# Performance work log

Hardware: AMD Instinct MI355X
Metric: run time of the kernel (lower is better)

The kernel has to match this reference:

```python
import jax, jax.numpy as jnp
import numpy as np

T, B, D, H = 512, 128, 512, 512

def setup_inputs() -> dict:
    key = jax.random.key(0)
    k1, k2, k3, k4 = jax.random.split(key, 4)
    s_in = 1.0 / np.sqrt(D)
    s_h = 1.0 / np.sqrt(H)
    return {
        "x": jax.random.normal(k1, (T, B, D), dtype=jnp.float32),
        "resets": jax.random.randint(k2, (T, B), 0, 2) > 0,
        "h0": jnp.zeros((B, H), dtype=jnp.float32),  # GRUCell.initialize_carry -> zeros
        "Wi": jax.random.normal(k3, (D, 3 * H), dtype=jnp.float32) * s_in,  # [ir|iz|in]
        "bi": jnp.zeros((3 * H,), dtype=jnp.float32),
        "Wh": jax.random.normal(k4, (H, 3 * H), dtype=jnp.float32) * s_h,  # [hr|hz|hn]
        "bhn": jnp.zeros((H,), dtype=jnp.float32),
    }

def reference(x, resets, h0, Wi, bi, Wh, bhn):
    # Precompute all input-side gate projections in one big GEMM: [T,B,3H]
    xg = jnp.einsum('tbd,dk->tbk', x, Wi) + bi

    def step(h, inp):
        xg_t, reset_t = inp
        # reset masking: replace carry with fresh zero carry where episode resets
        h = jnp.where(reset_t[:, None], jnp.zeros_like(h), h)
        hg = h @ Wh  # [B,3H]
        xr, xz, xn = jnp.split(xg_t, 3, axis=-1)
        hr, hz, hn = jnp.split(hg, 3, axis=-1)
        r = jax.nn.sigmoid(xr + hr)
        z = jax.nn.sigmoid(xz + hz)
        n = jnp.tanh(xn + r * (hn + bhn))
        h_new = (1.0 - z) * n + z * h
        return h_new, h_new

    h_final, ys = jax.lax.scan(step, h0, (xg, resets))
    return h_final, ys
```

## Files before the change

### kernel.cpp

```cpp
#include <hip/hip_runtime.h>

typedef __attribute__((ext_vector_type(4))) float f32x4;
typedef __attribute__((ext_vector_type(8))) _Float16 f16x8;
typedef __attribute__((ext_vector_type(4))) _Float16 f16x4;
typedef unsigned short u16;
typedef unsigned int u32;
typedef unsigned long long u64;

#define XGCAP 36864

__device__ __forceinline__ float sigm(float v){ return 1.0f / (1.0f + __expf(-v)); }
__device__ __forceinline__ float tanh_fast(float v){
  v = fminf(15.0f, fmaxf(-15.0f, v));
  float e = __expf(2.0f * v);
  return (e - 1.0f) / (e + 1.0f);
}
__device__ __forceinline__ void gload16(const void* g, void* l){
  __builtin_amdgcn_global_load_lds((const __attribute__((address_space(1))) void*)g,
                                   (__attribute__((address_space(3))) void*)l, 16, 0, 0);
}
__device__ __forceinline__ double aload(const double* p){
  return __hip_atomic_load(p, __ATOMIC_RELAXED, __HIP_MEMORY_SCOPE_AGENT);
}
__device__ __forceinline__ void astore(float* p, float v){
  __hip_atomic_store(p, v, __ATOMIC_RELAXED, __HIP_MEMORY_SCOPE_AGENT);
}
__device__ __forceinline__ float2 d2f2(double d){ union{double d; float2 f;} u; u.d = d; return u.f; }

__global__ __launch_bounds__(512) void prep_lists(
    const void* __restrict__ resets_raw,
    u32* __restrict__ rows, u32* __restrict__ off, int* __restrict__ nlists)
{
  __shared__ u32 bitmap[2048];
  __shared__ u32 cnt[520];
  __shared__ u32 offs[521];
  __shared__ u32 cur[520];
  __shared__ int is_bytes;
  const int tid = threadIdx.x;
  const int lane = tid & 63, wave = tid >> 6;
  for (int i = tid; i < 2048; i += 512) bitmap[i] = 0;
  for (int i = tid; i < 520; i += 512){ cnt[i] = 0; cur[i] = 0; }
  if (tid == 0) is_bytes = 0;
  for (int i = tid; i < 64; i += 512) rows[65536 + i] = (2u << 16);
  __syncthreads();
  {
    const u32* w = (const u32*)resets_raw;
    int bad = 0;
    for (int i = tid; i < 4096; i += 512) bad |= (w[i] > 1u);
    if (bad) atomicOr(&is_bytes, 1);
  }
  __syncthreads();
  if (is_bytes){
    const u32* wb = (const u32*)resets_raw;
    for (int i = tid; i < 16384; i += 512){
      u32 v = wb[i];
      u32 bits = ((v & 0xFFu) ? 1u : 0u) | (((v >> 8) & 0xFFu) ? 2u : 0u)
               | (((v >> 16) & 0xFFu) ? 4u : 0u) | (((v >> 24) & 0xFFu) ? 8u : 0u);
      if (bits) atomicOr(&bitmap[i >> 3], bits << ((i & 7) * 4));
    }
  } else {
    const u32* w = (const u32*)resets_raw;
    for (int r = 0; r < 128; ++r){
      u32 v = w[r * 512 + tid];
      u64 m = __ballot(v != 0u);
      if (lane == 0){
        int idx = r * 16 + wave * 2;
        bitmap[idx]     = (u32)m;
        bitmap[idx + 1] = (u32)(m >> 32);
      }
    }
  }
  __syncthreads();
  if (tid < 128){
    const int b = tid;
    int depth = 0;
    for (int t = 0; t < 512; ++t){
      int pos = t * 128 + b;
      bool rs = (bitmap[pos >> 5] >> (pos & 31)) & 1u;
      depth = rs ? 0 : ((t == 0) ? 0 : depth + 1);
      int li = (depth == 0) ? (rs ? 0 : 1) : (depth + 1);
      atomicAdd(&cnt[li], 1u);
    }
  }
  __syncthreads();
  if (tid == 0){
    u32 s = 0; int mx = 0;
    for (int i = 0; i < 520; ++i){
      offs[i] = s; s += cnt[i];
      if (cnt[i]) mx = i;
    }
    offs[520] = s;
    *nlists = mx + 1;
  }
  __syncthreads();
  for (int i = tid; i < 521; i += 512) off[i] = offs[i];
  __syncthreads();
  if (tid < 128){
    const int b = tid;
    int depth = 0;
    for (int t = 0; t < 512; ++t){
      int pos = t * 128 + b;
      bool rs = (bitmap[pos >> 5] >> (pos & 31)) & 1u;
      depth = rs ? 0 : ((t == 0) ? 0 : depth + 1);
      int li = (depth == 0) ? (rs ? 0 : 1) : (depth + 1);
      u32 p = offs[li] + atomicAdd(&cur[li], 1u);
      u32 fl = rs ? 1u : ((t == 0) ? 2u : 0u);
      rows[p] = (u32)t | ((u32)b << 9) | (fl << 16);
    }
  }
}

__global__ void prep_w(const float* __restrict__ Wi, const float* __restrict__ Wh,
                       char* __restrict__ wimg)
{
  __shared__ float tile[64][65];
  const int bc = blockIdx.x % 24;
  const int bk = blockIdx.x / 24;
  const int scol0 = (bc % 3) * 512 + (bc / 3) * 64;
  const int k0 = bk * 64;
  #pragma unroll
  for (int i = 0; i < 4; ++i){
    int idx = (int)threadIdx.x + i*256;
    int kk = idx >> 4, c4 = idx & 15;
    int k = k0 + kk;
    const float* src = (k < 512) ? (Wi + (size_t)k*1536 + scol0 + c4*4)
                                 : (Wh + (size_t)(k-512)*1536 + scol0 + c4*4);
    float4 v = *(const float4*)src;
    tile[kk][c4*4+0] = v.x; tile[kk][c4*4+1] = v.y;
    tile[kk][c4*4+2] = v.z; tile[kk][c4*4+3] = v.w;
  }
  __syncthreads();
  const int jb = bc / 3;
  #pragma unroll
  for (int i = 0; i < 4; ++i){
    int idx = (int)threadIdx.x + i*256;
    int cc = idx >> 4, k4 = idx & 15;
    int cimg = (bc % 3)*64 + cc;
    f16x4 c;
    c[0] = (_Float16)tile[k4*4+0][cc]; c[1] = (_Float16)tile[k4*4+1][cc];
    c[2] = (_Float16)tile[k4*4+2][cc]; c[3] = (_Float16)tile[k4*4+3][cc];
    int bby = k4*8;
    int sb = (bby & 8) | ((bby & 0x70) ^ ((cimg & 7) << 4));
    *(f16x4*)(wimg + ((size_t)(jb*16 + bk))*24576 + cimg*128 + sb) = c;
  }
}

__global__ __launch_bounds__(256, 2) void xg_gemm(
    const float* __restrict__ x, const float* __restrict__ bi,
    const float* __restrict__ bhn, const char* __restrict__ wimg,
    _Float16* __restrict__ xg, const u32* __restrict__ rows,
    const u32* __restrict__ off, u32* __restrict__ flags,
    float* __restrict__ out)
{
  __shared__ __align__(16) char smem[81920];
  const int tid = threadIdx.x;
  const int lane = tid & 63, wave = tid >> 6;
  const int c_  = (int)blockIdx.x & 7;
  const int q_  = (int)blockIdx.x >> 3;
  const int jblk = q_ & 7;
  const int tm = c_ + ((q_ >> 3) << 3);
  float* ys = out + 65536;
  const u32 n0 = off[1];
  const size_t wbase = ((size_t)jblk*16)*24576;

  const float* rp[8];
  #pragma unroll
  for (int i = 0; i < 8; ++i){
    u32 e = rows[tm*128 + (tid>>4) + i*16];
    rp[i] = x + ((size_t)((e & 511u)*128u + ((e >> 9) & 127u)))*512 + (tid & 15)*4;
  }

  f32x4 acc[3][8];
  #pragma unroll
  for (int c = 0; c < 3; ++c)
    #pragma unroll
    for (int m = 0; m < 8; ++m) acc[c][m] = (f32x4){0.f,0.f,0.f,0.f};

  float4 areg[8];
  #pragma unroll
  for (int i = 0; i < 8; ++i) areg[i] = *(const float4*)(rp[i]);
  {
    const char* g = wimg + wbase + wave*6144 + lane*16;
    char* l = smem + 32768 + wave*6144;
    #pragma unroll
    for (int i = 0; i < 6; ++i) gload16(g + i*1024, l + i*1024);
  }
  #pragma unroll
  for (int i = 0; i < 8; ++i){
    int r = (tid>>4) + i*16, bby = (tid & 15)*8;
    int sb = (bby & 8) | ((bby & 0x70) ^ ((r & 7) << 4));
    f16x4 c; c[0]=(_Float16)areg[i].x; c[1]=(_Float16)areg[i].y;
             c[2]=(_Float16)areg[i].z; c[3]=(_Float16)areg[i].w;
    *(f16x4*)(smem + r*128 + sb) = c;
  }
  __syncthreads();

  for (int kc = 0; kc < 8; ++kc){
    const int cur = kc & 1;
    if (kc < 7){
      #pragma unroll
      for (int i = 0; i < 8; ++i) areg[i] = *(const float4*)(rp[i] + (kc+1)*64);
      const char* g = wimg + wbase + (size_t)(kc+1)*24576 + wave*6144 + lane*16;
      char* l = smem + 32768 + ((kc+1)&1)*24576 + wave*6144;
      #pragma unroll
      for (int i = 0; i < 6; ++i) gload16(g + i*1024, l + i*1024);
    }
    const char* Ab = smem + cur*16384;
    const char* Wb = smem + 32768 + cur*24576;
    #pragma unroll
    for (int kk = 0; kk < 2; ++kk){
      const int bby = kk*64 + (lane>>4)*16;
      f16x8 af[8];
      #pragma unroll
      for (int mi = 0; mi < 8; ++mi){
        int rr = mi*16 + (lane & 15);
        af[mi] = *(const f16x8*)(Ab + rr*128 + (bby ^ ((rr & 7) << 4)));
      }
      #pragma unroll
      for (int cls = 0; cls < 3; ++cls){
        int cc = cls*64 + wave*16 + (lane & 15);
        f16x8 wf = *(const f16x8*)(Wb + cc*128 + (bby ^ ((cc & 7) << 4)));
        #pragma unroll
        for (int mi = 0; mi < 8; ++mi)
          acc[cls][mi] = __builtin_amdgcn_mfma_f32_16x16x32_f16(af[mi], wf, acc[cls][mi], 0, 0, 0);
      }
    }
    if (kc < 7){
      char* An = smem + ((kc+1)&1)*16384;
      #pragma unroll
      for (int i = 0; i < 8; ++i){
        int r = (tid>>4) + i*16, bby = (tid & 15)*8;
        int sb = (bby & 8) | ((bby & 0x70) ^ ((r & 7) << 4));
        f16x4 c; c[0]=(_Float16)areg[i].x; c[1]=(_Float16)areg[i].y;
                 c[2]=(_Float16)areg[i].z; c[3]=(_Float16)areg[i].w;
        *(f16x4*)(An + r*128 + sb) = c;
      }
    }
    __syncthreads();
  }

  const int jloc = wave*16 + (lane & 15);
  const int j = jblk*64 + jloc;
  const float bir = bi[j], biz = bi[512 + j], bin = bi[1024 + j], bh = bhn[j];
  #pragma unroll
  for (int mi = 0; mi < 8; ++mi){
    #pragma unroll
    for (int rg = 0; rg < 4; ++rg){
      int r = mi*16 + (lane >> 4)*4 + rg;
      u32 e = rows[tm*128 + r];
      int tt = (int)(e & 511u), bb = (int)((e >> 9) & 127u);
      float xr = acc[0][mi][rg] + bir;
      float xz = acc[1][mi][rg] + biz;
      float xn = acc[2][mi][rg] + bin;
      if ((e >> 16) == 1u){
        float rr = sigm(xr), zz = sigm(xz);
        float nn = tanh_fast(xn + rr*bh);
        ys[((size_t)(tt*128 + bb))*512 + j] = (1.f - zz)*nn;
      } else {
        u32 xi = (u32)(tm*128 + r) - n0;
        if (xi >= XGCAP) xi = 0;
        _Float16* p = xg + (size_t)xi*1536 + jblk*192 + jloc;
        p[0]   = (_Float16)xr;
        p[64]  = (_Float16)xz;
        p[128] = (_Float16)xn;
      }
    }
  }
  __syncthreads();
  if (tid < 128){
    u32 e = rows[tm*128 + tid];
    if ((e >> 16) == 1u){
      u32 fidx = (e & 511u)*128u + ((e >> 9) & 127u);
      __hip_atomic_fetch_add(&flags[fidx], 1u, __ATOMIC_RELAXED, __HIP_MEMORY_SCOPE_AGENT);
    }
  }
}

__global__ __launch_bounds__(256, 2) void gru_scan(
    const float* __restrict__ h0, const float* __restrict__ bhn,
    const char* __restrict__ wimg, const _Float16* __restrict__ xg,
    const u32* __restrict__ rows, const u32* __restrict__ off,
    const int* __restrict__ nlists, u32* __restrict__ flags,
    float* __restrict__ out)
{
  __shared__ __align__(16) char smem[32768];
  float* ys = out + 65536;
  const int L = *nlists;
  const u32 n0 = off[1];
  const int tid = threadIdx.x;
  const int lane = tid & 63, wave = tid >> 6;
  const int nblk = (int)gridDim.x;

  int myNext = (int)blockIdx.x;
  int gt = 0;
  for (int li = 1; li < L; ++li){
    const u32 offA = off[li];
    const int nA = (int)(off[li+1] - offA);
    const int tA = (nA + 63) >> 6;
    const int nt = tA * 8;
    while (myNext < gt + nt){
      const int tile = myNext - gt;
      myNext += nblk;
      const int tm = tile >> 3, jb = tile & 7;
      const u32 rowbase = offA + (u32)tm*64u;
      const int mcount = min(64, nA - tm*64);
      const char* wp = wimg + ((size_t)jb*16 + 8)*24576;
      const int jloc = wave*16 + (lane & 15);

      if (wave == 0){
        u32 e = rows[rowbase + lane];
        if (lane < mcount && (e >> 16) == 0u){
          u32 fidx = ((e & 511u) - 1u)*128u + ((e >> 9) & 127u);
          int guard = 0;
          while (__hip_atomic_load(&flags[fidx], __ATOMIC_RELAXED, __HIP_MEMORY_SCOPE_AGENT) < 8u){
            __builtin_amdgcn_s_sleep(1);
            if (++guard > (1 << 20)) break;
          }
        }
      }
      __syncthreads();

      const float* rp[4];
      #pragma unroll
      for (int i = 0; i < 4; ++i){
        u32 e = rows[rowbase + (tid>>4) + i*16];
        int tt = (int)(e & 511u), bb = (int)((e >> 9) & 127u);
        const float* base = ((e >> 16) == 0u) ? (ys + ((size_t)((tt-1)*128 + bb))*512)
                                              : (h0 + (size_t)bb*512);
        rp[i] = base + (tid & 15)*4;
      }

      _Float16 xgp[3][4][4];
      #pragma unroll
      for (int mi = 0; mi < 4; ++mi){
        #pragma unroll
        for (int rg = 0; rg < 4; ++rg){
          u32 lpos = rowbase + (u32)(mi*16 + (lane >> 4)*4 + rg);
          u32 xi = lpos - n0;
          if (xi >= XGCAP) xi = 0;
          const _Float16* p = xg + (size_t)xi*1536 + jb*192 + jloc;
          xgp[0][mi][rg] = p[0];
          xgp[1][mi][rg] = p[64];
          xgp[2][mi][rg] = p[128];
        }
      }

      f32x4 acc[3][4];
      #pragma unroll
      for (int c = 0; c < 3; ++c)
        #pragma unroll
        for (int m = 0; m < 4; ++m) acc[c][m] = (f32x4){0.f,0.f,0.f,0.f};
      float hp[4][4];
      double s0[4][2], s1[4][2], s2[4][2];

#define ALOAD(S, CK) do{ \
    _Pragma("unroll") for (int i_ = 0; i_ < 4; ++i_){ \
      const double* p_ = (const double*)(rp[i_] + (CK)*64); \
      S[i_][0] = aload(p_); S[i_][1] = aload(p_ + 1); } }while(0)

#define AWRITE(S, CK) do{ \
    char* An_ = smem + ((CK) & 3)*8192; \
    _Pragma("unroll") for (int i_ = 0; i_ < 4; ++i_){ \
      float2 u0_ = d2f2(S[i_][0]), u1_ = d2f2(S[i_][1]); \
      int r_ = (tid>>4) + i_*16, bby_ = (tid & 15)*8; \
      int sb_ = (bby_ & 8) | ((bby_ & 0x70) ^ ((r_ & 7) << 4)); \
      f16x4 c_; c_[0]=(_Float16)u0_.x; c_[1]=(_Float16)u0_.y; \
                c_[2]=(_Float16)u1_.x; c_[3]=(_Float16)u1_.y; \
      *(f16x4*)(An_ + r_*128 + sb_) = c_; } }while(0)

#define COMPUTE(KC) do{ \
    const char* Ab_ = smem + ((KC) & 3)*8192; \
    _Pragma("unroll") for (int kk_ = 0; kk_ < 2; ++kk_){ \
      const int bby_ = kk_*64 + (lane>>4)*16; \
      f16x8 af_[4]; \
      _Pragma("unroll") for (int mi_ = 0; mi_ < 4; ++mi_){ \
        int rr_ = mi_*16 + (lane & 15); \
        af_[mi_] = *(const f16x8*)(Ab_ + rr_*128 + (bby_ ^ ((rr_ & 7) << 4))); } \
      _Pragma("unroll") for (int cl_ = 0; cl_ < 3; ++cl_){ \
        int cc_ = cl_*64 + wave*16 + (lane & 15); \
        f16x8 wf_ = *(const f16x8*)(wp + (size_t)(KC)*24576 + cc_*128 + (bby_ ^ ((cc_ & 7) << 4))); \
        _Pragma("unroll") for (int mi_ = 0; mi_ < 4; ++mi_) \
          acc[cl_][mi_] = __builtin_amdgcn_mfma_f32_16x16x32_f16(af_[mi_], wf_, acc[cl_][mi_], 0, 0, 0); } } \
    if ((KC) == jb){ \
      const int bb2_ = jloc*2; \
      _Pragma("unroll") for (int mi_ = 0; mi_ < 4; ++mi_) \
        _Pragma("unroll") for (int rg_ = 0; rg_ < 4; ++rg_){ \
          int r2_ = mi_*16 + (lane >> 4)*4 + rg_; \
          int sb2_ = (bb2_ & 0x0F) | ((bb2_ & 0x70) ^ ((r2_ & 7) << 4)); \
          hp[mi_][rg_] = (float)(*(const _Float16*)(Ab_ + r2_*128 + sb2_)); } } }while(0)

      ALOAD(s0, 0); ALOAD(s1, 1); ALOAD(s2, 2);
      AWRITE(s0, 0);
      __syncthreads();
      ALOAD(s0, 3); COMPUTE(0); AWRITE(s1, 1); __syncthreads();
      ALOAD(s1, 4); COMPUTE(1); AWRITE(s2, 2); __syncthreads();
      ALOAD(s2, 5); COMPUTE(2); AWRITE(s0, 3); __syncthreads();
      ALOAD(s0, 6); COMPUTE(3); AWRITE(s1, 4); __syncthreads();
      ALOAD(s1, 7); COMPUTE(4); AWRITE(s2, 5); __syncthreads();
                    COMPUTE(5); AWRITE(s0, 6); __syncthreads();
                    COMPUTE(6); AWRITE(s1, 7); __syncthreads();
                    COMPUTE(7);
#undef ALOAD
#undef AWRITE
#undef COMPUTE

      const int j = jb*64 + jloc;
      const float bh = bhn[j];
      #pragma unroll
      for (int mi = 0; mi < 4; ++mi){
        #pragma unroll
        for (int rg = 0; rg < 4; ++rg){
          int r = mi*16 + (lane >> 4)*4 + rg;
          if (r < mcount){
            u32 e = rows[rowbase + r];
            int tt = (int)(e & 511u), bb = (int)((e >> 9) & 127u);
            float rr = sigm((float)xgp[0][mi][rg] + acc[0][mi][rg]);
            float zz = sigm((float)xgp[1][mi][rg] + acc[1][mi][rg]);
            float nn = tanh_fast((float)xgp[2][mi][rg] + rr*(acc[2][mi][rg] + bh));
            astore(&ys[((size_t)(tt*128 + bb))*512 + j], (1.f - zz)*nn + zz*hp[mi][rg]);
          }
        }
      }
      __syncthreads();
      if (tid < mcount){
        u32 e = rows[rowbase + tid];
        u32 fidx = (e & 511u)*128u + ((e >> 9) & 127u);
        __hip_atomic_fetch_add(&flags[fidx], 1u, __ATOMIC_RELAXED, __HIP_MEMORY_SCOPE_AGENT);
      }
    }
    gt += nt;
  }

  for (int v = (int)blockIdx.x; v < 512; v += nblk){
    const int b = v & 127, jq = v >> 7;
    if (tid == 0){
      int guard = 0;
      while (__hip_atomic_load(&flags[511*128 + b], __ATOMIC_RELAXED, __HIP_MEMORY_SCOPE_AGENT) < 8u){
        __builtin_amdgcn_s_sleep(1);
        if (++guard > (1 << 20)) break;
      }
    }
    __syncthreads();
    if (tid < 128){
      const float* src = &ys[((size_t)(511*128 + b))*512 + jq*128 + tid];
      float val = __hip_atomic_load(src, __ATOMIC_RELAXED, __HIP_MEMORY_SCOPE_AGENT);
      out[(size_t)b*512 + jq*128 + tid] = val;
    }
    __syncthreads();
  }
}

extern "C" void kernel_launch(void* const* d_in, const int* in_sizes, int n_in,
                              void* d_out, int out_size, void* d_ws, size_t ws_size,
                              hipStream_t stream)
{
  const float* x  = (const float*)d_in[0];
  const void*  resets = d_in[1];
  const float* h0 = (const float*)d_in[2];
  const float* Wi = (const float*)d_in[3];
  const float* bi = (const float*)d_in[4];
  const float* Wh = (const float*)d_in[5];
  const float* bhn= (const float*)d_in[6];
  float* out = (float*)d_out;

  char* ws = (char*)d_ws;
  u32* off    = (u32*)ws;
  int* nlists = (int*)(ws + 4096);
  u32* rows   = (u32*)(ws + 8192);
  u32* flags  = (u32*)(ws + 294912);
  char* wimg  = ws + 589824;
  _Float16* xg = (_Float16*)(ws + 4194304);

  hipMemsetAsync(flags, 0, 65536*sizeof(u32), stream);
  prep_lists<<<dim3(1), dim3(512), 0, stream>>>(resets, rows, off, nlists);
  prep_w<<<dim3(384), dim3(256), 0, stream>>>(Wi, Wh, wimg);
  xg_gemm<<<dim3(4096), dim3(256), 0, stream>>>(x, bi, bhn, wimg, xg, rows, off, flags, out);

  int perCU = 0;
  (void)hipOccupancyMaxActiveBlocksPerMultiprocessor(&perCU, gru_scan, 256, 0);
  if (perCU < 1) perCU = 1;
  int grid = perCU * 256;
  if (grid > 1024) grid = 1024;

  void* args[] = {(void*)&h0, (void*)&bhn, (void*)&wimg, (void*)&xg,
                  (void*)&rows, (void*)&off, (void*)&nlists, (void*)&flags, (void*)&out};
  hipLaunchCooperativeKernel(gru_scan, dim3(grid), dim3(256), args, 0, stream);

  (void)in_sizes; (void)n_in; (void)out_size; (void)ws_size;
}
```

Baseline: 921.4 us.

## Stage hidden states as packed fp16 in successor-ordered buffer for scan GEMM

Adds a successor index per scheduled row so each step writes its new hidden state, as fp16, straight into a dense buffer laid out in the consumer row order. The scan then loads the previous state with contiguous 8-byte loads and copies it to LDS without an fp32-to-fp16 conversion, instead of gathering scattered fp32 rows from ys/h0. It also folds t=0 rows into the reset list when h0 is all zeros, moves the flag clear from a memset into prep_w, and simplifies the xg_gemm tile order. The cost is extra writes of the fp16 state, a serial h0 scan in prep_lists, and a much larger workspace.

```diff
diff --git a/kernel.cpp b/kernel.cpp
--- a/kernel.cpp
+++ b/kernel.cpp
@@ -7,7 +7,8 @@
 typedef unsigned int u32;
 typedef unsigned long long u64;
 
-#define XGCAP 36864
+#define XGCAP 34304
+#define TRASH (XGCAP - 1)
 
 __device__ __forceinline__ float sigm(float v){ return 1.0f / (1.0f + __expf(-v)); }
 __device__ __forceinline__ float tanh_fast(float v){
@@ -25,22 +26,26 @@
 __device__ __forceinline__ void astore(float* p, float v){
   __hip_atomic_store(p, v, __ATOMIC_RELAXED, __HIP_MEMORY_SCOPE_AGENT);
 }
-__device__ __forceinline__ float2 d2f2(double d){ union{double d; float2 f;} u; u.d = d; return u.f; }
+__device__ __forceinline__ void astore16(u16* p, u16 v){
+  __hip_atomic_store(p, v, __ATOMIC_RELAXED, __HIP_MEMORY_SCOPE_AGENT);
+}
+__device__ __forceinline__ u16 h2b(_Float16 h){ union{_Float16 h; u16 u;} c; c.h = h; return c.u; }
 
 __global__ __launch_bounds__(512) void prep_lists(
-    const void* __restrict__ resets_raw,
-    u32* __restrict__ rows, u32* __restrict__ off, int* __restrict__ nlists)
+    const void* __restrict__ resets_raw, const float* __restrict__ h0,
+    u32* __restrict__ rows, u32* __restrict__ off, int* __restrict__ nlists,
+    u32* __restrict__ succ, _Float16* __restrict__ hq)
 {
   __shared__ u32 bitmap[2048];
   __shared__ u32 cnt[520];
   __shared__ u32 offs[521];
   __shared__ u32 cur[520];
-  __shared__ int is_bytes;
+  __shared__ int is_bytes, h0nz;
   const int tid = threadIdx.x;
   const int lane = tid & 63, wave = tid >> 6;
   for (int i = tid; i < 2048; i += 512) bitmap[i] = 0;
   for (int i = tid; i < 520; i += 512){ cnt[i] = 0; cur[i] = 0; }
-  if (tid == 0) is_bytes = 0;
+  if (tid == 0){ is_bytes = 0; h0nz = 0; }
   for (int i = tid; i < 64; i += 512) rows[65536 + i] = (2u << 16);
   __syncthreads();
   {
@@ -49,7 +54,14 @@
     for (int i = tid; i < 4096; i += 512) bad |= (w[i] > 1u);
     if (bad) atomicOr(&is_bytes, 1);
   }
-  __syncthreads();
+  {
+    const u32* hw = (const u32*)h0;
+    u32 o = 0;
+    for (int i = tid; i < 65536; i += 512) o |= hw[i];
+    if (o) atomicOr(&h0nz, 1);
+  }
+  __syncthreads();
+  const bool h0zero = (h0nz == 0);
   if (is_bytes){
     const u32* wb = (const u32*)resets_raw;
     for (int i = tid; i < 16384; i += 512){
@@ -65,8 +77,7 @@
       u64 m = __ballot(v != 0u);
       if (lane == 0){
         int idx = r * 16 + wave * 2;
-        bitmap[idx]     = (u32)m;
-        bitmap[idx + 1] = (u32)(m >> 32);
+        bitmap[idx] = (u32)m; bitmap[idx + 1] = (u32)(m >> 32);
       }
     }
   }
@@ -78,7 +89,7 @@
       int pos = t * 128 + b;
       bool rs = (bitmap[pos >> 5] >> (pos & 31)) & 1u;
       depth = rs ? 0 : ((t == 0) ? 0 : depth + 1);
-      int li = (depth == 0) ? (rs ? 0 : 1) : (depth + 1);
+      int li = (depth == 0) ? ((rs || h0zero) ? 0 : 1) : (depth + 1);
       atomicAdd(&cnt[li], 1u);
     }
   }
@@ -95,24 +106,44 @@
   __syncthreads();
   for (int i = tid; i < 521; i += 512) off[i] = offs[i];
   __syncthreads();
+  const u32 n0 = offs[1];
   if (tid < 128){
     const int b = tid;
     int depth = 0;
+    u32 prev_p = 0;
     for (int t = 0; t < 512; ++t){
       int pos = t * 128 + b;
       bool rs = (bitmap[pos >> 5] >> (pos & 31)) & 1u;
       depth = rs ? 0 : ((t == 0) ? 0 : depth + 1);
-      int li = (depth == 0) ? (rs ? 0 : 1) : (depth + 1);
+      int li = (depth == 0) ? ((rs || h0zero) ? 0 : 1) : (depth + 1);
       u32 p = offs[li] + atomicAdd(&cur[li], 1u);
-      u32 fl = rs ? 1u : ((t == 0) ? 2u : 0u);
+      u32 fl = rs ? 1u : ((t == 0) ? (h0zero ? 1u : 2u) : 0u);
       rows[p] = (u32)t | ((u32)b << 9) | (fl << 16);
+      succ[p] = TRASH;
+      if (t > 0 && !rs) succ[prev_p] = p - n0;
+      prev_p = p;
+    }
+  }
+  __syncthreads();
+  if (!h0zero){
+    const u32 c1 = offs[2] - offs[1];
+    for (u32 idx = tid; idx < c1 * 512u; idx += 512){
+      u32 lpos = offs[1] + (idx >> 9);
+      u32 c = idx & 511u;
+      u32 b = (rows[lpos] >> 9) & 127u;
+      hq[(size_t)(lpos - n0) * 512 + c] = (_Float16)h0[(size_t)b * 512 + c];
     }
   }
 }
 
 __global__ void prep_w(const float* __restrict__ Wi, const float* __restrict__ Wh,
-                       char* __restrict__ wimg)
+                       char* __restrict__ wimg, u32* __restrict__ flags)
 {
+  if (blockIdx.x < 64){
+    #pragma unroll
+    for (int i = 0; i < 4; ++i)
+      flags[blockIdx.x * 1024 + (int)threadIdx.x + i * 256] = 0;
+  }
   __shared__ float tile[64][65];
   const int bc = blockIdx.x % 24;
   const int bk = blockIdx.x / 24;
@@ -149,16 +180,14 @@
     const float* __restrict__ x, const float* __restrict__ bi,
     const float* __restrict__ bhn, const char* __restrict__ wimg,
     _Float16* __restrict__ xg, const u32* __restrict__ rows,
-    const u32* __restrict__ off, u32* __restrict__ flags,
+    const u32* __restrict__ off, const u32* __restrict__ succ,
+    _Float16* __restrict__ hq, u32* __restrict__ flags,
     float* __restrict__ out)
 {
   __shared__ __align__(16) char smem[81920];
   const int tid = threadIdx.x;
   const int lane = tid & 63, wave = tid >> 6;
-  const int c_  = (int)blockIdx.x & 7;
-  const int q_  = (int)blockIdx.x >> 3;
-  const int jblk = q_ & 7;
-  const int tm = c_ + ((q_ >> 3) << 3);
+  const int tm = (int)blockIdx.x >> 3, jblk = (int)blockIdx.x & 7;
   float* ys = out + 65536;
   const u32 n0 = off[1];
   const size_t wbase = ((size_t)jblk*16)*24576;
@@ -255,7 +284,10 @@
       if ((e >> 16) == 1u){
         float rr = sigm(xr), zz = sigm(xz);
         float nn = tanh_fast(xn + rr*bh);
-        ys[((size_t)(tt*128 + bb))*512 + j] = (1.f - zz)*nn;
+        float hv = (1.f - zz)*nn;
+        ys[((size_t)(tt*128 + bb))*512 + j] = hv;
+        u32 sx = succ[tm*128 + r];
+        hq[(size_t)sx*512 + j] = (_Float16)hv;
       } else {
         u32 xi = (u32)(tm*128 + r) - n0;
         if (xi >= XGCAP) xi = 0;
@@ -277,11 +309,11 @@
 }
 
 __global__ __launch_bounds__(256, 2) void gru_scan(
-    const float* __restrict__ h0, const float* __restrict__ bhn,
-    const char* __restrict__ wimg, const _Float16* __restrict__ xg,
+    const float* __restrict__ bhn, const char* __restrict__ wimg,
+    const _Float16* __restrict__ xg, _Float16* __restrict__ hq,
     const u32* __restrict__ rows, const u32* __restrict__ off,
-    const int* __restrict__ nlists, u32* __restrict__ flags,
-    float* __restrict__ out)
+    const int* __restrict__ nlists, const u32* __restrict__ succ,
+    u32* __restrict__ flags, float* __restrict__ out)
 {
   __shared__ __align__(16) char smem[32768];
   float* ys = out + 65536;
@@ -290,6 +322,7 @@
   const int tid = threadIdx.x;
   const int lane = tid & 63, wave = tid >> 6;
   const int nblk = (int)gridDim.x;
+  const double* hqd = (const double*)hq;
 
   int myNext = (int)blockIdx.x;
   int gt = 0;
@@ -303,6 +336,7 @@
       myNext += nblk;
       const int tm = tile >> 3, jb = tile & 7;
       const u32 rowbase = offA + (u32)tm*64u;
+      const u32 xibase = rowbase - n0;
       const int mcount = min(64, nA - tm*64);
       const char* wp = wimg + ((size_t)jb*16 + 8)*24576;
       const int jloc = wave*16 + (lane & 15);
@@ -320,23 +354,12 @@
       }
       __syncthreads();
 
-      const float* rp[4];
-      #pragma unroll
-      for (int i = 0; i < 4; ++i){
-        u32 e = rows[rowbase + (tid>>4) + i*16];
-        int tt = (int)(e & 511u), bb = (int)((e >> 9) & 127u);
-        const float* base = ((e >> 16) == 0u) ? (ys + ((size_t)((tt-1)*128 + bb))*512)
-                                              : (h0 + (size_t)bb*512);
-        rp[i] = base + (tid & 15)*4;
-      }
-
       _Float16 xgp[3][4][4];
       #pragma unroll
       for (int mi = 0; mi < 4; ++mi){
         #pragma unroll
         for (int rg = 0; rg < 4; ++rg){
-          u32 lpos = rowbase + (u32)(mi*16 + (lane >> 4)*4 + rg);
-          u32 xi = lpos - n0;
+          u32 xi = xibase + (u32)(mi*16 + (lane >> 4)*4 + rg);
           if (xi >= XGCAP) xi = 0;
           const _Float16* p = xg + (size_t)xi*1536 + jb*192 + jloc;
           xgp[0][mi][rg] = p[0];
@@ -351,22 +374,19 @@
         #pragma unroll
         for (int m = 0; m < 4; ++m) acc[c][m] = (f32x4){0.f,0.f,0.f,0.f};
       float hp[4][4];
-      double s0[4][2], s1[4][2], s2[4][2];
+      double s0[4], s1[4], s2[4];
 
 #define ALOAD(S, CK) do{ \
-    _Pragma("unroll") for (int i_ = 0; i_ < 4; ++i_){ \
-      const double* p_ = (const double*)(rp[i_] + (CK)*64); \
-      S[i_][0] = aload(p_); S[i_][1] = aload(p_ + 1); } }while(0)
+    const double* p_ = hqd + (size_t)(xibase + (u32)(tid>>2))*128 + (CK)*16 + (tid&3)*4; \
+    S[0] = aload(p_); S[1] = aload(p_+1); S[2] = aload(p_+2); S[3] = aload(p_+3); }while(0)
 
 #define AWRITE(S, CK) do{ \
     char* An_ = smem + ((CK) & 3)*8192; \
+    int r_ = tid>>2; \
     _Pragma("unroll") for (int i_ = 0; i_ < 4; ++i_){ \
-      float2 u0_ = d2f2(S[i_][0]), u1_ = d2f2(S[i_][1]); \
-      int r_ = (tid>>4) + i_*16, bby_ = (tid & 15)*8; \
+      int bby_ = (tid&3)*32 + i_*8; \
       int sb_ = (bby_ & 8) | ((bby_ & 0x70) ^ ((r_ & 7) << 4)); \
-      f16x4 c_; c_[0]=(_Float16)u0_.x; c_[1]=(_Float16)u0_.y; \
-                c_[2]=(_Float16)u1_.x; c_[3]=(_Float16)u1_.y; \
-      *(f16x4*)(An_ + r_*128 + sb_) = c_; } }while(0)
+      *(double*)(An_ + r_*128 + sb_) = S[i_]; } }while(0)
 
 #define COMPUTE(KC) do{ \
     const char* Ab_ = smem + ((KC) & 3)*8192; \
@@ -417,7 +437,10 @@
             float rr = sigm((float)xgp[0][mi][rg] + acc[0][mi][rg]);
             float zz = sigm((float)xgp[1][mi][rg] + acc[1][mi][rg]);
             float nn = tanh_fast((float)xgp[2][mi][rg] + rr*(acc[2][mi][rg] + bh));
-            astore(&ys[((size_t)(tt*128 + bb))*512 + j], (1.f - zz)*nn + zz*hp[mi][rg]);
+            float hv = (1.f - zz)*nn + zz*hp[mi][rg];
+            astore(&ys[((size_t)(tt*128 + bb))*512 + j], hv);
+            u32 sx = succ[rowbase + r];
+            astore16((u16*)hq + (size_t)sx*512 + j, h2b((_Float16)hv));
           }
         }
       }
@@ -468,13 +491,14 @@
   int* nlists = (int*)(ws + 4096);
   u32* rows   = (u32*)(ws + 8192);
   u32* flags  = (u32*)(ws + 294912);
-  char* wimg  = ws + 589824;
+  u32* succ   = (u32*)(ws + 589824);
+  char* wimg  = ws + 917504;
   _Float16* xg = (_Float16*)(ws + 4194304);
-
-  hipMemsetAsync(flags, 0, 65536*sizeof(u32), stream);
-  prep_lists<<<dim3(1), dim3(512), 0, stream>>>(resets, rows, off, nlists);
-  prep_w<<<dim3(384), dim3(256), 0, stream>>>(Wi, Wh, wimg);
-  xg_gemm<<<dim3(4096), dim3(256), 0, stream>>>(x, bi, bhn, wimg, xg, rows, off, flags, out);
+  _Float16* hq = (_Float16*)(ws + 109576192);
+
+  prep_lists<<<dim3(1), dim3(512), 0, stream>>>(resets, h0, rows, off, nlists, succ, hq);
+  prep_w<<<dim3(384), dim3(256), 0, stream>>>(Wi, Wh, wimg, flags);
+  xg_gemm<<<dim3(4096), dim3(256), 0, stream>>>(x, bi, bhn, wimg, xg, rows, off, succ, hq, flags, out);
 
   int perCU = 0;
   (void)hipOccupancyMaxActiveBlocksPerMultiprocessor(&perCU, gru_scan, 256, 0);
@@ -482,8 +506,9 @@
   int grid = perCU * 256;
   if (grid > 1024) grid = 1024;
 
-  void* args[] = {(void*)&h0, (void*)&bhn, (void*)&wimg, (void*)&xg,
-                  (void*)&rows, (void*)&off, (void*)&nlists, (void*)&flags, (void*)&out};
+  void* args[] = {(void*)&bhn, (void*)&wimg, (void*)&xg, (void*)&hq,
+                  (void*)&rows, (void*)&off, (void*)&nlists, (void*)&succ,
+                  (void*)&flags, (void*)&out};
   hipLaunchCooperativeKernel(gru_scan, dim3(grid), dim3(256), args, 0, stream);
 
   (void)in_sizes; (void)n_in; (void)out_size; (void)ws_size;
```

After: 1.275 ms. +38.4%, slower.
